# Kernel tuning notes

Hardware: AMD Instinct MI355X
Metric: run time of the kernel (lower is better)

## Reference

```python
import jax, jax.numpy as jnp
import numpy as np

OBS_DIM, EMBED_DIM, HIDDEN = 64, 128, 256
BATCH, SEQLEN = 32, 2048


def setup_inputs() -> dict:
    key = jax.random.key(0)
    ks = jax.random.split(key, 8)
    N = BATCH * SEQLEN
    obs = jax.random.normal(ks[0], (N, OBS_DIM), dtype=jnp.float32)
    S = jnp.zeros((BATCH, 2 * HIDDEN), dtype=jnp.float32)  # [h, c] concat
    M = (jax.random.uniform(ks[1], (N,)) < 0.1).astype(jnp.float32)
    sc_e = 1.0 / np.sqrt(OBS_DIM)
    sc_k = 1.0 / np.sqrt(EMBED_DIM)
    sc_r = 1.0 / np.sqrt(HIDDEN)
    W_embed = jax.random.normal(ks[2], (OBS_DIM, EMBED_DIM), dtype=jnp.float32) * sc_e
    b_embed = jnp.zeros((EMBED_DIM,), dtype=jnp.float32)
    kernel = jax.random.normal(ks[3], (EMBED_DIM, 4 * HIDDEN), dtype=jnp.float32) * sc_k
    rec_kernel = jax.random.normal(ks[4], (HIDDEN, 4 * HIDDEN), dtype=jnp.float32) * sc_r
    bias = jnp.zeros((4 * HIDDEN,), dtype=jnp.float32)
    return {"obs": obs, "S": S, "M": M, "W_embed": W_embed, "b_embed": b_embed,
            "kernel": kernel, "rec_kernel": rec_kernel, "bias": bias}


def reference(obs, S, M, W_embed, b_embed, kernel, rec_kernel, bias):
    B = S.shape[0]
    H = S.shape[1] // 2
    # embedding_model: Dense  [B*T, obs_dim] -> [B*T, embed_dim]
    emb = obs @ W_embed + b_embed
    T = emb.shape[0] // B
    x = emb.reshape(B, T, -1)          # batch_to_seq
    m = M.reshape(B, T)                # batch_to_seq of mask
    h0, c0 = jnp.split(S, 2, axis=-1)  # LSTM states [h, c]

    def step(carry, xt):
        h, c = carry
        x_t, m_t = xt                  # x_t: [B, D], m_t: [B]
        keep = (1.0 - m_t)[:, None]    # mask==1 -> reset state (episode boundary)
        h = h * keep
        c = c * keep
        z = x_t @ kernel + h @ rec_kernel + bias  # [B, 4H]
        i, f, g, o = jnp.split(z, 4, axis=-1)     # keras gate order i,f,c,o
        i = jax.nn.sigmoid(i)
        f = jax.nn.sigmoid(f)
        g = jnp.tanh(g)
        o = jax.nn.sigmoid(o)
        c = f * c + i * g
        h = o * jnp.tanh(c)
        return (h, c), h

    xs = (jnp.swapaxes(x, 0, 1), jnp.swapaxes(m, 0, 1))  # time-major
    (_, _), hs = jax.lax.scan(step, (h0, c0), xs)        # hs: [T, B, H]
    memory = jnp.swapaxes(hs, 0, 1).reshape(B * T, H)    # seq_to_batch
    return memory
```

## Files before the change

kernel.cpp:

```cpp
#include <hip/hip_runtime.h>
#include <hip/hip_bf16.h>


#define T_SEQ   2048
#define NBATCH  32
#define OBS     64
#define HID     256
#define KROWS   320
#define GSLOTS  16
#define XPAD    324
#define MAXSEG  65536

__device__ __forceinline__ float sigm(float x) {
    x = fminf(fmaxf(x, -30.f), 30.f);
    return 1.f / (1.f + __expf(-x));
}
__device__ __forceinline__ float tanh_(float x) {
    x = fminf(fmaxf(x, -15.f), 15.f);
    float e = __expf(2.f * x);
    return (e - 1.f) / (e + 1.f);
}

__global__ void prep_kernel(const float* __restrict__ W_embed, const float* __restrict__ b_embed,
                            const float* __restrict__ kern,    const float* __restrict__ rec,
                            const float* __restrict__ bias,
                            float* __restrict__ Wg, float* __restrict__ bc4, unsigned* __restrict__ cnt) {
    int bi = blockIdx.x, tid = threadIdx.x;
    if (bi < 256) {
        int r = bi >> 2;
        int c = ((bi & 3) << 8) + tid;
        float acc = 0.f;
        #pragma unroll 8
        for (int k = 0; k < 128; ++k)
            acc = fmaf(W_embed[r * 128 + k], kern[k * 1024 + c], acc);
        Wg[(r * 256 + (c & 255)) * 4 + (c >> 8)] = acc;
    } else if (bi < 512) {
        int k = bi - 256;
        #pragma unroll
        for (int p = 0; p < 4; ++p) {
            int c = (p << 8) + tid;
            Wg[((64 + k) * 256 + (c & 255)) * 4 + (c >> 8)] = rec[k * 1024 + c];
        }
    } else if (bi == 512) {
        #pragma unroll
        for (int p = 0; p < 4; ++p) {
            int c = (p << 8) + tid;
            float acc = bias[c];
            for (int k = 0; k < 128; ++k)
                acc = fmaf(b_embed[k], kern[k * 1024 + c], acc);
            bc4[(c & 255) * 4 + (c >> 8)] = acc;
        }
    } else {
        if (tid < 16) cnt[tid] = 0u;
    }
}

__global__ void seg_kernel(const float* __restrict__ M, uint2* __restrict__ segs,
                           unsigned* __restrict__ cnt) {
    int b = blockIdx.x, tid = threadIdx.x;
    int base = b * T_SEQ;
    for (int t = tid; t < T_SEQ; t += 256) {
        bool start = (t == 0) || (M[base + t] != 0.f);
        if (!start) continue;
        int t2 = t + 1;
        while (t2 < T_SEQ && M[base + t2] == 0.f) ++t2;
        unsigned idx = atomicAdd(&cnt[0], 1u);
        segs[idx] = make_uint2((unsigned)(base + t), (unsigned)(t2 - t));
    }
}

__global__ void sort_kernel(const uint2* __restrict__ segs, uint2* __restrict__ out,
                            unsigned* __restrict__ cnt) {
    __shared__ unsigned hist[2049];
    __shared__ unsigned partial[256];
    __shared__ unsigned ofs[2049];
    int tid = threadIdx.x;
    unsigned n = cnt[0];
    for (int i = tid; i < 2049; i += 256) hist[i] = 0u;
    __syncthreads();
    for (unsigned i = tid; i < n; i += 256) atomicAdd(&hist[segs[i].y], 1u);
    __syncthreads();
    int cs = tid * 8 + 1;
    unsigned s = 0;
    #pragma unroll
    for (int i = 0; i < 8; ++i) s += hist[cs + i];
    partial[tid] = s;
    __syncthreads();
    if (tid == 0) {
        unsigned run = 0;
        for (int t = 255; t >= 0; --t) { unsigned p = partial[t]; partial[t] = run; run += p; }
    }
    __syncthreads();
    unsigned run = partial[tid];
    #pragma unroll
    for (int i = 7; i >= 0; --i) { int bin = cs + i; ofs[bin] = run; run += hist[bin]; }
    __syncthreads();
    for (unsigned i = tid; i < n; i += 256) {
        uint2 sg = segs[i];
        unsigned pos = atomicAdd(&ofs[sg.y], 1u);
        out[pos] = sg;
    }
}

template <int N>
__device__ __forceinline__ void step_n(float (*X)[XPAD], float (*C)[HID],
                                       const float* __restrict__ Wg,
                                       const float* __restrict__ bc4,
                                       const unsigned* __restrict__ ssn,
                                       float* __restrict__ out, int tid) {
    const float4* __restrict__ W4 = (const float4*)Wg;
    float4 acc[N];
    const float4 bcv = ((const float4*)bc4)[tid];
    #pragma unroll
    for (int g = 0; g < N; ++g) acc[g] = bcv;

    for (int k4 = 0; k4 < KROWS / 4; ++k4) {
        float4 w[4];
        #pragma unroll
        for (int i = 0; i < 4; ++i) w[i] = W4[(k4 * 4 + i) * 256 + tid];
        #pragma unroll
        for (int g = 0; g < N; ++g) {
            const float4 xv = *(const float4*)&X[g][k4 * 4];
            float xs0 = xv.x, xs1 = xv.y, xs2 = xv.z, xs3 = xv.w;
            acc[g].x = fmaf(xs0, w[0].x, acc[g].x);
            acc[g].y = fmaf(xs0, w[0].y, acc[g].y);
            acc[g].z = fmaf(xs0, w[0].z, acc[g].z);
            acc[g].w = fmaf(xs0, w[0].w, acc[g].w);
            acc[g].x = fmaf(xs1, w[1].x, acc[g].x);
            acc[g].y = fmaf(xs1, w[1].y, acc[g].y);
            acc[g].z = fmaf(xs1, w[1].z, acc[g].z);
            acc[g].w = fmaf(xs1, w[1].w, acc[g].w);
            acc[g].x = fmaf(xs2, w[2].x, acc[g].x);
            acc[g].y = fmaf(xs2, w[2].y, acc[g].y);
            acc[g].z = fmaf(xs2, w[2].z, acc[g].z);
            acc[g].w = fmaf(xs2, w[2].w, acc[g].w);
            acc[g].x = fmaf(xs3, w[3].x, acc[g].x);
            acc[g].y = fmaf(xs3, w[3].y, acc[g].y);
            acc[g].z = fmaf(xs3, w[3].z, acc[g].z);
            acc[g].w = fmaf(xs3, w[3].w, acc[g].w);
        }
    }
    float hv[N], cv[N];
    #pragma unroll
    for (int g = 0; g < N; ++g) {
        float i = sigm(acc[g].x);
        float f = sigm(acc[g].y);
        float gg = tanh_(acc[g].z);
        float o = sigm(acc[g].w);
        float c = fmaf(f, C[g][tid], i * gg);
        hv[g] = o * tanh_(c);
        cv[g] = c;
    }
    __syncthreads();
    #pragma unroll
    for (int g = 0; g < N; ++g) {
        C[g][tid] = cv[g];
        X[g][OBS + tid] = hv[g];
        out[(size_t)ssn[g] * HID + tid] = hv[g];
    }
}

__launch_bounds__(256)
__global__ void lstm_kernel(const float* __restrict__ obs, const float* __restrict__ S,
                            const float* __restrict__ M,
                            const float* __restrict__ Wg, const float* __restrict__ bc4,
                            const uint2* __restrict__ segs, unsigned* __restrict__ cnt,
                            float* __restrict__ out) {
    __shared__ float X[GSLOTS][XPAD];
    __shared__ float C[GSLOTS][HID];
    __shared__ unsigned ssn[GSLOTS], send[GSLOTS];
    __shared__ int   sact[GSLOTS], sfresh[GSLOTS];
    __shared__ float smg[GSLOTS];
    __shared__ int   sh_nact, sh_nmig;
    __shared__ unsigned sh_mask;
    __shared__ int   msrc[GSLOTS], mdst[GSLOTS];

    const int tid = threadIdx.x;
    const unsigned nseg = cnt[0];
    if (tid < GSLOTS) sact[tid] = 0;
    __syncthreads();

    for (;;) {
        if (tid < GSLOTS) {
            int g = tid;
            if (sact[g]) {
                unsigned nn = ssn[g] + 1;
                if (nn >= send[g]) sact[g] = 0; else ssn[g] = nn;
            }
            sfresh[g] = 0;
            if (!sact[g]) {
                unsigned idx = atomicAdd(&cnt[1], 1u);
                if (idx < nseg) {
                    uint2 sg = segs[idx];
                    ssn[g] = sg.x; send[g] = sg.x + sg.y;
                    sact[g] = 1; sfresh[g] = 1;
                }
            }
        }
        if (tid < 64) {
            unsigned long long bal = __ballot(tid < GSLOTS && sact[tid]);
            if (tid == 0) {
                unsigned m = (unsigned)(bal & 0xFFFFull);
                sh_mask = m;
                sh_nact = __popc(m);
            }
        }
        __syncthreads();
        const unsigned mask = sh_mask;
        if (mask == 0u) break;
        const int nact = sh_nact;

        if (mask != ((1u << nact) - 1u)) {
            if (tid == 0) {
                int w = 0, nm = 0;
                for (int g = 0; g < GSLOTS; ++g) if (sact[g]) {
                    if (g != w) {
                        msrc[nm] = g; mdst[nm] = w; ++nm;
                        ssn[w] = ssn[g]; send[w] = send[g];
                        sfresh[w] = sfresh[g];
                        sact[w] = 1; sact[g] = 0;
                    }
                    ++w;
                }
                sh_nmig = nm;
            }
            __syncthreads();
            const int nm = sh_nmig;
            for (int i = 0; i < nm; ++i) {
                int s = msrc[i], d = mdst[i];
                X[d][tid] = X[s][tid];
                if (tid + 256 < XPAD) X[d][tid + 256] = X[s][tid + 256];
                C[d][tid] = C[s][tid];
            }
            __syncthreads();
        }

        if (tid < GSLOTS) {
            int g = tid;
            smg[g] = (g < nact) ? M[ssn[g]] : 0.f;
        }
        for (int g = 0; g < nact; ++g) {
            if (sfresh[g]) {
                unsigned n0 = ssn[g];
                if ((n0 & (T_SEQ - 1)) == 0u) {
                    unsigned b = n0 >> 11;
                    X[g][OBS + tid] = S[b * 512 + tid];
                    C[g][tid]       = S[b * 512 + 256 + tid];
                } else {
                    X[g][OBS + tid] = 0.f;
                    C[g][tid]       = 0.f;
                }
            }
        }
        {
            int g = (tid >> 6);
            int e = tid & 63;
            #pragma unroll
            for (int p = 0; p < 4; ++p, g += 4)
                if (g < nact) X[g][e] = obs[(size_t)ssn[g] * OBS + e];
        }
        __syncthreads();

        for (int g = 0; g < nact; ++g) {
            if (smg[g] != 0.f) { X[g][OBS + tid] = 0.f; C[g][tid] = 0.f; }
        }
        __syncthreads();

        switch (nact) {
            case 1:  step_n<1>(X, C, Wg, bc4, ssn, out, tid); break;
            case 2:  step_n<2>(X, C, Wg, bc4, ssn, out, tid); break;
            case 3:  step_n<3>(X, C, Wg, bc4, ssn, out, tid); break;
            case 4:  step_n<4>(X, C, Wg, bc4, ssn, out, tid); break;
            case 5:  step_n<5>(X, C, Wg, bc4, ssn, out, tid); break;
            case 6:  step_n<6>(X, C, Wg, bc4, ssn, out, tid); break;
            case 7:  step_n<7>(X, C, Wg, bc4, ssn, out, tid); break;
            case 8:  step_n<8>(X, C, Wg, bc4, ssn, out, tid); break;
            case 9:  step_n<9>(X, C, Wg, bc4, ssn, out, tid); break;
            case 10: step_n<10>(X, C, Wg, bc4, ssn, out, tid); break;
            case 11: step_n<11>(X, C, Wg, bc4, ssn, out, tid); break;
            case 12: step_n<12>(X, C, Wg, bc4, ssn, out, tid); break;
            case 13: step_n<13>(X, C, Wg, bc4, ssn, out, tid); break;
            case 14: step_n<14>(X, C, Wg, bc4, ssn, out, tid); break;
            case 15: step_n<15>(X, C, Wg, bc4, ssn, out, tid); break;
            default: step_n<16>(X, C, Wg, bc4, ssn, out, tid); break;
        }
        __syncthreads();
    }
}

extern "C" void kernel_launch(void* const* d_in, const int* in_sizes, int n_in,
                              void* d_out, int out_size, void* d_ws, size_t ws_size,
                              hipStream_t stream) {
    const float* obs     = (const float*)d_in[0];
    const float* S       = (const float*)d_in[1];
    const float* M       = (const float*)d_in[2];
    const float* W_embed = (const float*)d_in[3];
    const float* b_embed = (const float*)d_in[4];
    const float* kern    = (const float*)d_in[5];
    const float* rec     = (const float*)d_in[6];
    const float* bias    = (const float*)d_in[7];
    float* out = (float*)d_out;

    float*    ws    = (float*)d_ws;
    float*    Wg    = ws;
    float*    bc4   = Wg + 320 * 1024;
    unsigned* cnt   = (unsigned*)(bc4 + 1024);
    uint2*    segs  = (uint2*)(cnt + 16);
    uint2*    ssort = segs + MAXSEG;

    hipLaunchKernelGGL(prep_kernel, dim3(514), dim3(256), 0, stream,
                       W_embed, b_embed, kern, rec, bias, Wg, bc4, cnt);
    hipLaunchKernelGGL(seg_kernel, dim3(NBATCH), dim3(256), 0, stream, M, segs, cnt);
    hipLaunchKernelGGL(sort_kernel, dim3(1), dim3(256), 0, stream, segs, ssort, cnt);
    hipLaunchKernelGGL(lstm_kernel, dim3(256), dim3(256), 0, stream,
                       obs, S, M, Wg, bc4, ssort, cnt, out);
}
```

Baseline: 3.010 ms.

## Keep fp16-packed LSTM weights in registers, one segment per 1024-thread block

Rewrites the LSTM kernel so each of 1024 threads owns one gate column and holds its 320 weights as 160 packed fp16 pairs in registers. Each block processes one segment at a time with fp16 dot2 instructions, replacing the multi-slot batching scheme that re-read fp32 weights from global/L2 every step. Weights and hidden state are quantised to fp16, which reduces precision. The 160-register weight array with launch_bounds(1024,8) risks register spills, and processing a single segment per step gives up the batching across segments.

```diff
diff --git a/kernel.cpp b/kernel.cpp
--- a/kernel.cpp
+++ b/kernel.cpp
@@ -1,5 +1,6 @@
 #include <hip/hip_runtime.h>
 #include <hip/hip_bf16.h>
+#include <hip/hip_fp16.h>
 
 
 #define T_SEQ   2048
@@ -7,9 +8,9 @@
 #define OBS     64
 #define HID     256
 #define KROWS   320
-#define GSLOTS  16
-#define XPAD    324
+#define KP      160
 #define MAXSEG  65536
+#define NWG     512
 
 __device__ __forceinline__ float sigm(float x) {
     x = fminf(fmaxf(x, -30.f), 30.f);
@@ -21,37 +22,52 @@
     return (e - 1.f) / (e + 1.f);
 }
 
+typedef _Float16 h2_t __attribute__((ext_vector_type(2)));
+__device__ __forceinline__ float dot2(unsigned w, unsigned x, float acc) {
+#if defined(__has_builtin) && __has_builtin(__builtin_amdgcn_fdot2)
+    return __builtin_amdgcn_fdot2(__builtin_bit_cast(h2_t, w),
+                                  __builtin_bit_cast(h2_t, x), acc, false);
+#else
+    float wl = __half2float(__ushort_as_half((unsigned short)(w & 0xffffu)));
+    float wh = __half2float(__ushort_as_half((unsigned short)(w >> 16)));
+    float xl = __half2float(__ushort_as_half((unsigned short)(x & 0xffffu)));
+    float xh = __half2float(__ushort_as_half((unsigned short)(x >> 16)));
+    return fmaf(wh, xh, fmaf(wl, xl, acc));
+#endif
+}
+
+__device__ __forceinline__ unsigned packh(float a, float b) {
+    return (unsigned)__half_as_ushort(__float2half(a)) |
+           ((unsigned)__half_as_ushort(__float2half(b)) << 16);
+}
+
 __global__ void prep_kernel(const float* __restrict__ W_embed, const float* __restrict__ b_embed,
                             const float* __restrict__ kern,    const float* __restrict__ rec,
                             const float* __restrict__ bias,
-                            float* __restrict__ Wg, float* __restrict__ bc4, unsigned* __restrict__ cnt) {
-    int bi = blockIdx.x, tid = threadIdx.x;
-    if (bi < 256) {
-        int r = bi >> 2;
-        int c = ((bi & 3) << 8) + tid;
-        float acc = 0.f;
+                            unsigned* __restrict__ Wp, float* __restrict__ bc,
+                            unsigned* __restrict__ cnt) {
+    int kp = blockIdx.x, j = threadIdx.x;
+    if (kp < 32) {
+        int r0 = 2 * kp, r1 = 2 * kp + 1;
+        float wa = 0.f, wb = 0.f;
         #pragma unroll 8
+        for (int k = 0; k < 128; ++k) {
+            float kv = kern[k * 1024 + j];
+            wa = fmaf(W_embed[r0 * 128 + k], kv, wa);
+            wb = fmaf(W_embed[r1 * 128 + k], kv, wb);
+        }
+        Wp[kp * 1024 + j] = packh(wa, wb);
+    } else if (kp < 160) {
+        int k0 = 2 * (kp - 32);
+        float wa = rec[(size_t)k0 * 1024 + j];
+        float wb = rec[(size_t)(k0 + 1) * 1024 + j];
+        Wp[kp * 1024 + j] = packh(wa, wb);
+    } else {
+        float acc = bias[j];
         for (int k = 0; k < 128; ++k)
-            acc = fmaf(W_embed[r * 128 + k], kern[k * 1024 + c], acc);
-        Wg[(r * 256 + (c & 255)) * 4 + (c >> 8)] = acc;
-    } else if (bi < 512) {
-        int k = bi - 256;
-        #pragma unroll
-        for (int p = 0; p < 4; ++p) {
-            int c = (p << 8) + tid;
-            Wg[((64 + k) * 256 + (c & 255)) * 4 + (c >> 8)] = rec[k * 1024 + c];
-        }
-    } else if (bi == 512) {
-        #pragma unroll
-        for (int p = 0; p < 4; ++p) {
-            int c = (p << 8) + tid;
-            float acc = bias[c];
-            for (int k = 0; k < 128; ++k)
-                acc = fmaf(b_embed[k], kern[k * 1024 + c], acc);
-            bc4[(c & 255) * 4 + (c >> 8)] = acc;
-        }
-    } else {
-        if (tid < 16) cnt[tid] = 0u;
+            acc = fmaf(b_embed[k], kern[k * 1024 + j], acc);
+        bc[j] = acc;
+        if (j < 16) cnt[j] = 0u;
     }
 }
 
@@ -102,189 +118,75 @@
     }
 }
 
-template <int N>
-__device__ __forceinline__ void step_n(float (*X)[XPAD], float (*C)[HID],
-                                       const float* __restrict__ Wg,
-                                       const float* __restrict__ bc4,
-                                       const unsigned* __restrict__ ssn,
-                                       float* __restrict__ out, int tid) {
-    const float4* __restrict__ W4 = (const float4*)Wg;
-    float4 acc[N];
-    const float4 bcv = ((const float4*)bc4)[tid];
-    #pragma unroll
-    for (int g = 0; g < N; ++g) acc[g] = bcv;
-
-    for (int k4 = 0; k4 < KROWS / 4; ++k4) {
-        float4 w[4];
-        #pragma unroll
-        for (int i = 0; i < 4; ++i) w[i] = W4[(k4 * 4 + i) * 256 + tid];
-        #pragma unroll
-        for (int g = 0; g < N; ++g) {
-            const float4 xv = *(const float4*)&X[g][k4 * 4];
-            float xs0 = xv.x, xs1 = xv.y, xs2 = xv.z, xs3 = xv.w;
-            acc[g].x = fmaf(xs0, w[0].x, acc[g].x);
-            acc[g].y = fmaf(xs0, w[0].y, acc[g].y);
-            acc[g].z = fmaf(xs0, w[0].z, acc[g].z);
-            acc[g].w = fmaf(xs0, w[0].w, acc[g].w);
-            acc[g].x = fmaf(xs1, w[1].x, acc[g].x);
-            acc[g].y = fmaf(xs1, w[1].y, acc[g].y);
-            acc[g].z = fmaf(xs1, w[1].z, acc[g].z);
-            acc[g].w = fmaf(xs1, w[1].w, acc[g].w);
-            acc[g].x = fmaf(xs2, w[2].x, acc[g].x);
-            acc[g].y = fmaf(xs2, w[2].y, acc[g].y);
-            acc[g].z = fmaf(xs2, w[2].z, acc[g].z);
-            acc[g].w = fmaf(xs2, w[2].w, acc[g].w);
-            acc[g].x = fmaf(xs3, w[3].x, acc[g].x);
-            acc[g].y = fmaf(xs3, w[3].y, acc[g].y);
-            acc[g].z = fmaf(xs3, w[3].z, acc[g].z);
-            acc[g].w = fmaf(xs3, w[3].w, acc[g].w);
-        }
-    }
-    float hv[N], cv[N];
-    #pragma unroll
-    for (int g = 0; g < N; ++g) {
-        float i = sigm(acc[g].x);
-        float f = sigm(acc[g].y);
-        float gg = tanh_(acc[g].z);
-        float o = sigm(acc[g].w);
-        float c = fmaf(f, C[g][tid], i * gg);
-        hv[g] = o * tanh_(c);
-        cv[g] = c;
-    }
-    __syncthreads();
-    #pragma unroll
-    for (int g = 0; g < N; ++g) {
-        C[g][tid] = cv[g];
-        X[g][OBS + tid] = hv[g];
-        out[(size_t)ssn[g] * HID + tid] = hv[g];
-    }
-}
-
-__launch_bounds__(256)
-__global__ void lstm_kernel(const float* __restrict__ obs, const float* __restrict__ S,
-                            const float* __restrict__ M,
-                            const float* __restrict__ Wg, const float* __restrict__ bc4,
-                            const uint2* __restrict__ segs, unsigned* __restrict__ cnt,
-                            float* __restrict__ out) {
-    __shared__ float X[GSLOTS][XPAD];
-    __shared__ float C[GSLOTS][HID];
-    __shared__ unsigned ssn[GSLOTS], send[GSLOTS];
-    __shared__ int   sact[GSLOTS], sfresh[GSLOTS];
-    __shared__ float smg[GSLOTS];
-    __shared__ int   sh_nact, sh_nmig;
-    __shared__ unsigned sh_mask;
-    __shared__ int   msrc[GSLOTS], mdst[GSLOTS];
+__global__ __launch_bounds__(1024, 8)
+void lstm_kernel(const float* __restrict__ obs, const float* __restrict__ S,
+                 const float* __restrict__ M,
+                 const unsigned* __restrict__ Wp, const float* __restrict__ bc,
+                 const uint2* __restrict__ segs, unsigned* __restrict__ cnt,
+                 float* __restrict__ out) {
+    __shared__ uint4 X4[KP / 4];
+    __shared__ float zb[1024];
+    __shared__ unsigned sh_idx;
+    __half* Xh = (__half*)X4;
 
     const int tid = threadIdx.x;
     const unsigned nseg = cnt[0];
-    if (tid < GSLOTS) sact[tid] = 0;
-    __syncthreads();
-
+
+    unsigned w[KP];
+    {
+        const unsigned* wp = Wp + tid;
+        #pragma unroll
+        for (int kp = 0; kp < KP; ++kp) w[kp] = wp[kp << 10];
+    }
+    const float bcj = bc[tid];
+
+    float c = 0.f;
     for (;;) {
-        if (tid < GSLOTS) {
-            int g = tid;
-            if (sact[g]) {
-                unsigned nn = ssn[g] + 1;
-                if (nn >= send[g]) sact[g] = 0; else ssn[g] = nn;
+        if (tid == 0) sh_idx = atomicAdd(&cnt[1], 1u);
+        __syncthreads();
+        unsigned idx = sh_idx;
+        if (idx >= nseg) break;
+        uint2 sg = segs[idx];
+        unsigned n0 = sg.x, n1 = sg.x + sg.y;
+
+        if (tid < HID) {
+            float h0 = 0.f;
+            c = 0.f;
+            if ((n0 & (T_SEQ - 1)) == 0u && M[n0] == 0.f) {
+                unsigned b = n0 >> 11;
+                h0 = S[b * 512 + tid];
+                c  = S[b * 512 + 256 + tid];
             }
-            sfresh[g] = 0;
-            if (!sact[g]) {
-                unsigned idx = atomicAdd(&cnt[1], 1u);
-                if (idx < nseg) {
-                    uint2 sg = segs[idx];
-                    ssn[g] = sg.x; send[g] = sg.x + sg.y;
-                    sact[g] = 1; sfresh[g] = 1;
-                }
+            Xh[OBS + tid] = __float2half(h0);
+        }
+
+        for (unsigned n = n0; n < n1; ++n) {
+            if (tid < OBS) Xh[tid] = __float2half(obs[(size_t)n * OBS + tid]);
+            __syncthreads();
+            float a0 = bcj, a1 = 0.f, a2 = 0.f, a3 = 0.f;
+            #pragma unroll
+            for (int q = 0; q < KP / 4; ++q) {
+                uint4 xv = X4[q];
+                a0 = dot2(w[q * 4 + 0], xv.x, a0);
+                a1 = dot2(w[q * 4 + 1], xv.y, a1);
+                a2 = dot2(w[q * 4 + 2], xv.z, a2);
+                a3 = dot2(w[q * 4 + 3], xv.w, a3);
+            }
+            zb[tid] = (a0 + a1) + (a2 + a3);
+            __syncthreads();
+            if (tid < HID) {
+                float zi = zb[tid], zf = zb[tid + 256];
+                float zg = zb[tid + 512], zo = zb[tid + 768];
+                float i = sigm(zi);
+                float f = sigm(zf);
+                float g = tanh_(zg);
+                float o = sigm(zo);
+                c = fmaf(f, c, i * g);
+                float h = o * tanh_(c);
+                Xh[OBS + tid] = __float2half(h);
+                out[(size_t)n * HID + tid] = h;
             }
         }
-        if (tid < 64) {
-            unsigned long long bal = __ballot(tid < GSLOTS && sact[tid]);
-            if (tid == 0) {
-                unsigned m = (unsigned)(bal & 0xFFFFull);
-                sh_mask = m;
-                sh_nact = __popc(m);
-            }
-        }
-        __syncthreads();
-        const unsigned mask = sh_mask;
-        if (mask == 0u) break;
-        const int nact = sh_nact;
-
-        if (mask != ((1u << nact) - 1u)) {
-            if (tid == 0) {
-                int w = 0, nm = 0;
-                for (int g = 0; g < GSLOTS; ++g) if (sact[g]) {
-                    if (g != w) {
-                        msrc[nm] = g; mdst[nm] = w; ++nm;
-                        ssn[w] = ssn[g]; send[w] = send[g];
-                        sfresh[w] = sfresh[g];
-                        sact[w] = 1; sact[g] = 0;
-                    }
-                    ++w;
-                }
-                sh_nmig = nm;
-            }
-            __syncthreads();
-            const int nm = sh_nmig;
-            for (int i = 0; i < nm; ++i) {
-                int s = msrc[i], d = mdst[i];
-                X[d][tid] = X[s][tid];
-                if (tid + 256 < XPAD) X[d][tid + 256] = X[s][tid + 256];
-                C[d][tid] = C[s][tid];
-            }
-            __syncthreads();
-        }
-
-        if (tid < GSLOTS) {
-            int g = tid;
-            smg[g] = (g < nact) ? M[ssn[g]] : 0.f;
-        }
-        for (int g = 0; g < nact; ++g) {
-            if (sfresh[g]) {
-                unsigned n0 = ssn[g];
-                if ((n0 & (T_SEQ - 1)) == 0u) {
-                    unsigned b = n0 >> 11;
-                    X[g][OBS + tid] = S[b * 512 + tid];
-                    C[g][tid]       = S[b * 512 + 256 + tid];
-                } else {
-                    X[g][OBS + tid] = 0.f;
-                    C[g][tid]       = 0.f;
-                }
-            }
-        }
-        {
-            int g = (tid >> 6);
-            int e = tid & 63;
-            #pragma unroll
-            for (int p = 0; p < 4; ++p, g += 4)
-                if (g < nact) X[g][e] = obs[(size_t)ssn[g] * OBS + e];
-        }
-        __syncthreads();
-
-        for (int g = 0; g < nact; ++g) {
-            if (smg[g] != 0.f) { X[g][OBS + tid] = 0.f; C[g][tid] = 0.f; }
-        }
-        __syncthreads();
-
-        switch (nact) {
-            case 1:  step_n<1>(X, C, Wg, bc4, ssn, out, tid); break;
-            case 2:  step_n<2>(X, C, Wg, bc4, ssn, out, tid); break;
-            case 3:  step_n<3>(X, C, Wg, bc4, ssn, out, tid); break;
-            case 4:  step_n<4>(X, C, Wg, bc4, ssn, out, tid); break;
-            case 5:  step_n<5>(X, C, Wg, bc4, ssn, out, tid); break;
-            case 6:  step_n<6>(X, C, Wg, bc4, ssn, out, tid); break;
-            case 7:  step_n<7>(X, C, Wg, bc4, ssn, out, tid); break;
-            case 8:  step_n<8>(X, C, Wg, bc4, ssn, out, tid); break;
-            case 9:  step_n<9>(X, C, Wg, bc4, ssn, out, tid); break;
-            case 10: step_n<10>(X, C, Wg, bc4, ssn, out, tid); break;
-            case 11: step_n<11>(X, C, Wg, bc4, ssn, out, tid); break;
-            case 12: step_n<12>(X, C, Wg, bc4, ssn, out, tid); break;
-            case 13: step_n<13>(X, C, Wg, bc4, ssn, out, tid); break;
-            case 14: step_n<14>(X, C, Wg, bc4, ssn, out, tid); break;
-            case 15: step_n<15>(X, C, Wg, bc4, ssn, out, tid); break;
-            default: step_n<16>(X, C, Wg, bc4, ssn, out, tid); break;
-        }
-        __syncthreads();
     }
 }
 
@@ -301,17 +203,16 @@
     const float* bias    = (const float*)d_in[7];
     float* out = (float*)d_out;
 
-    float*    ws    = (float*)d_ws;
-    float*    Wg    = ws;
-    float*    bc4   = Wg + 320 * 1024;
-    unsigned* cnt   = (unsigned*)(bc4 + 1024);
+    unsigned* Wp    = (unsigned*)d_ws;
+    float*    bc    = (float*)(Wp + KP * 1024);
+    unsigned* cnt   = (unsigned*)(bc + 1024);
     uint2*    segs  = (uint2*)(cnt + 16);
     uint2*    ssort = segs + MAXSEG;
 
-    hipLaunchKernelGGL(prep_kernel, dim3(514), dim3(256), 0, stream,
-                       W_embed, b_embed, kern, rec, bias, Wg, bc4, cnt);
+    hipLaunchKernelGGL(prep_kernel, dim3(161), dim3(1024), 0, stream,
+                       W_embed, b_embed, kern, rec, bias, Wp, bc, cnt);
     hipLaunchKernelGGL(seg_kernel, dim3(NBATCH), dim3(256), 0, stream, M, segs, cnt);
     hipLaunchKernelGGL(sort_kernel, dim3(1), dim3(256), 0, stream, segs, ssort, cnt);
-    hipLaunchKernelGGL(lstm_kernel, dim3(256), dim3(256), 0, stream,
-                       obs, S, M, Wg, bc4, ssort, cnt, out);
-}
+    hipLaunchKernelGGL(lstm_kernel, dim3(NWG), dim3(1024), 0, stream,
+                       obs, S, M, Wp, bc, ssort, cnt, out);
+}
```

Result: slower. 5.062 ms (+68.2%).

## Pack weights to fp16 with dot2, precompute input projection, keep cell state in registers

Applied to the files above, without the earlier changes.

Stores the fused embed/kernel and recurrent weights as packed fp16 pairs. Per-step gate accumulation now uses fdot2 instructions, which halves weight bandwidth and instruction count. A new zx_kernel precomputes the input-side projection for all timesteps into an fp16 workspace buffer when workspace space allows, so the recurrent loop only handles the 256 hidden rows. The cell state moves from shared memory into registers, the reset mask is folded into segment starts, and the grid doubles to 512 workgroups with 2 blocks per CU. The trade-off is reduced numeric precision (fp16 weights, inputs and h) and a dependence on workspace size.

```diff
diff --git a/kernel.cpp b/kernel.cpp
--- a/kernel.cpp
+++ b/kernel.cpp
@@ -1,15 +1,17 @@
 #include <hip/hip_runtime.h>
 #include <hip/hip_bf16.h>
+#include <hip/hip_fp16.h>
 
 
 #define T_SEQ   2048
 #define NBATCH  32
 #define OBS     64
 #define HID     256
-#define KROWS   320
 #define GSLOTS  16
-#define XPAD    324
+#define NK2     160
+#define ZK2     32
 #define MAXSEG  65536
+#define NWG     512
 
 __device__ __forceinline__ float sigm(float x) {
     x = fminf(fmaxf(x, -30.f), 30.f);
@@ -21,37 +23,94 @@
     return (e - 1.f) / (e + 1.f);
 }
 
+typedef _Float16 h2_t __attribute__((ext_vector_type(2)));
+__device__ __forceinline__ float dot2(unsigned w, unsigned x, float acc) {
+#if defined(__has_builtin) && __has_builtin(__builtin_amdgcn_fdot2)
+    return __builtin_amdgcn_fdot2(__builtin_bit_cast(h2_t, w),
+                                  __builtin_bit_cast(h2_t, x), acc, false);
+#else
+    float wl = __half2float(__ushort_as_half((unsigned short)(w & 0xffffu)));
+    float wh = __half2float(__ushort_as_half((unsigned short)(w >> 16)));
+    float xl = __half2float(__ushort_as_half((unsigned short)(x & 0xffffu)));
+    float xh = __half2float(__ushort_as_half((unsigned short)(x >> 16)));
+    return fmaf(wh, xh, fmaf(wl, xl, acc));
+#endif
+}
+__device__ __forceinline__ unsigned packh(float a, float b) {
+    return (unsigned)__half_as_ushort(__float2half(a)) |
+           ((unsigned)__half_as_ushort(__float2half(b)) << 16);
+}
+
 __global__ void prep_kernel(const float* __restrict__ W_embed, const float* __restrict__ b_embed,
                             const float* __restrict__ kern,    const float* __restrict__ rec,
                             const float* __restrict__ bias,
-                            float* __restrict__ Wg, float* __restrict__ bc4, unsigned* __restrict__ cnt) {
-    int bi = blockIdx.x, tid = threadIdx.x;
-    if (bi < 256) {
-        int r = bi >> 2;
-        int c = ((bi & 3) << 8) + tid;
-        float acc = 0.f;
-        #pragma unroll 8
-        for (int k = 0; k < 128; ++k)
-            acc = fmaf(W_embed[r * 128 + k], kern[k * 1024 + c], acc);
-        Wg[(r * 256 + (c & 255)) * 4 + (c >> 8)] = acc;
-    } else if (bi < 512) {
-        int k = bi - 256;
-        #pragma unroll
-        for (int p = 0; p < 4; ++p) {
-            int c = (p << 8) + tid;
-            Wg[((64 + k) * 256 + (c & 255)) * 4 + (c >> 8)] = rec[k * 1024 + c];
-        }
-    } else if (bi == 512) {
-        #pragma unroll
-        for (int p = 0; p < 4; ++p) {
-            int c = (p << 8) + tid;
-            float acc = bias[c];
-            for (int k = 0; k < 128; ++k)
-                acc = fmaf(b_embed[k], kern[k * 1024 + c], acc);
-            bc4[(c & 255) * 4 + (c >> 8)] = acc;
-        }
+                            uint4* __restrict__ W4, float4* __restrict__ bc4,
+                            unsigned* __restrict__ cnt) {
+    int b = blockIdx.x, j = threadIdx.x;
+    if (b < ZK2) {
+        int r0 = 2 * b, r1 = r0 + 1;
+        float d0[4] = {0.f, 0.f, 0.f, 0.f}, d1[4] = {0.f, 0.f, 0.f, 0.f};
+        for (int k = 0; k < 128; ++k) {
+            float e0 = W_embed[r0 * 128 + k], e1 = W_embed[r1 * 128 + k];
+            #pragma unroll
+            for (int q = 0; q < 4; ++q) {
+                float kv = kern[k * 1024 + (q << 8) + j];
+                d0[q] = fmaf(e0, kv, d0[q]);
+                d1[q] = fmaf(e1, kv, d1[q]);
+            }
+        }
+        W4[b * 256 + j] = make_uint4(packh(d0[0], d1[0]), packh(d0[1], d1[1]),
+                                     packh(d0[2], d1[2]), packh(d0[3], d1[3]));
+    } else if (b < NK2) {
+        size_t k0 = (size_t)2 * (b - ZK2), k1 = k0 + 1;
+        W4[b * 256 + j] = make_uint4(
+            packh(rec[k0 * 1024 + j],       rec[k1 * 1024 + j]),
+            packh(rec[k0 * 1024 + 256 + j], rec[k1 * 1024 + 256 + j]),
+            packh(rec[k0 * 1024 + 512 + j], rec[k1 * 1024 + 512 + j]),
+            packh(rec[k0 * 1024 + 768 + j], rec[k1 * 1024 + 768 + j]));
     } else {
-        if (tid < 16) cnt[tid] = 0u;
+        float a[4];
+        #pragma unroll
+        for (int q = 0; q < 4; ++q) a[q] = bias[(q << 8) + j];
+        for (int k = 0; k < 128; ++k) {
+            float e = b_embed[k];
+            #pragma unroll
+            for (int q = 0; q < 4; ++q)
+                a[q] = fmaf(e, kern[k * 1024 + (q << 8) + j], a[q]);
+        }
+        bc4[j] = make_float4(a[0], a[1], a[2], a[3]);
+        if (j < 16) cnt[j] = 0u;
+    }
+}
+
+__global__ __launch_bounds__(256, 2)
+void zx_kernel(const float* __restrict__ obs, const uint4* __restrict__ W4,
+               const float4* __restrict__ bc4, uint2* __restrict__ zx4) {
+    __shared__ __half obsh[64][64];
+    const int tid = threadIdx.x;
+    const size_t base = (size_t)blockIdx.x * 64 * 64;
+    const size_t row0 = (size_t)blockIdx.x * 64;
+    for (int i = tid; i < 4096; i += 256)
+        obsh[i >> 6][i & 63] = __float2half(obs[base + i]);
+    __syncthreads();
+
+    uint4 w[32];
+    #pragma unroll
+    for (int k2 = 0; k2 < 32; ++k2) w[k2] = W4[k2 * 256 + tid];
+    const float4 bc = bc4[tid];
+
+    const unsigned* __restrict__ ob32 = (const unsigned*)obsh;
+    for (int n = 0; n < 64; ++n) {
+        float4 a = bc;
+        #pragma unroll
+        for (int k2 = 0; k2 < 32; ++k2) {
+            unsigned xv = ob32[n * 32 + k2];
+            a.x = dot2(w[k2].x, xv, a.x);
+            a.y = dot2(w[k2].y, xv, a.y);
+            a.z = dot2(w[k2].z, xv, a.z);
+            a.w = dot2(w[k2].w, xv, a.w);
+        }
+        zx4[(row0 + n) * 256 + tid] = make_uint2(packh(a.x, a.y), packh(a.z, a.w));
     }
 }
 
@@ -102,81 +161,91 @@
     }
 }
 
-template <int N>
-__device__ __forceinline__ void step_n(float (*X)[XPAD], float (*C)[HID],
-                                       const float* __restrict__ Wg,
-                                       const float* __restrict__ bc4,
-                                       const unsigned* __restrict__ ssn,
-                                       float* __restrict__ out, int tid) {
-    const float4* __restrict__ W4 = (const float4*)Wg;
+template <int N, int Z0>
+__device__ __forceinline__ void step_n(unsigned (*X)[NK2], float (&c)[GSLOTS],
+                                       const uint4* __restrict__ W4,
+                                       const float4* __restrict__ bc4,
+                                       const uint2* __restrict__ zx4,
+                                       const unsigned* ssn, float* __restrict__ out,
+                                       int tid) {
     float4 acc[N];
-    const float4 bcv = ((const float4*)bc4)[tid];
-    #pragma unroll
-    for (int g = 0; g < N; ++g) acc[g] = bcv;
-
-    for (int k4 = 0; k4 < KROWS / 4; ++k4) {
-        float4 w[4];
-        #pragma unroll
-        for (int i = 0; i < 4; ++i) w[i] = W4[(k4 * 4 + i) * 256 + tid];
+    if (Z0 == 0) {
+        const float4 b = bc4[tid];
+        #pragma unroll
+        for (int g = 0; g < N; ++g) acc[g] = b;
+    } else {
         #pragma unroll
         for (int g = 0; g < N; ++g) {
-            const float4 xv = *(const float4*)&X[g][k4 * 4];
-            float xs0 = xv.x, xs1 = xv.y, xs2 = xv.z, xs3 = xv.w;
-            acc[g].x = fmaf(xs0, w[0].x, acc[g].x);
-            acc[g].y = fmaf(xs0, w[0].y, acc[g].y);
-            acc[g].z = fmaf(xs0, w[0].z, acc[g].z);
-            acc[g].w = fmaf(xs0, w[0].w, acc[g].w);
-            acc[g].x = fmaf(xs1, w[1].x, acc[g].x);
-            acc[g].y = fmaf(xs1, w[1].y, acc[g].y);
-            acc[g].z = fmaf(xs1, w[1].z, acc[g].z);
-            acc[g].w = fmaf(xs1, w[1].w, acc[g].w);
-            acc[g].x = fmaf(xs2, w[2].x, acc[g].x);
-            acc[g].y = fmaf(xs2, w[2].y, acc[g].y);
-            acc[g].z = fmaf(xs2, w[2].z, acc[g].z);
-            acc[g].w = fmaf(xs2, w[2].w, acc[g].w);
-            acc[g].x = fmaf(xs3, w[3].x, acc[g].x);
-            acc[g].y = fmaf(xs3, w[3].y, acc[g].y);
-            acc[g].z = fmaf(xs3, w[3].z, acc[g].z);
-            acc[g].w = fmaf(xs3, w[3].w, acc[g].w);
-        }
-    }
-    float hv[N], cv[N];
+            uint2 z = zx4[(size_t)ssn[g] * 256 + tid];
+            acc[g].x = __half2float(__ushort_as_half((unsigned short)(z.x & 0xffffu)));
+            acc[g].y = __half2float(__ushort_as_half((unsigned short)(z.x >> 16)));
+            acc[g].z = __half2float(__ushort_as_half((unsigned short)(z.y & 0xffffu)));
+            acc[g].w = __half2float(__ushort_as_half((unsigned short)(z.y >> 16)));
+        }
+    }
+    for (int k2 = Z0; k2 < NK2; k2 += 4) {
+        uint4 w0 = W4[(k2 + 0) * 256 + tid];
+        uint4 w1 = W4[(k2 + 1) * 256 + tid];
+        uint4 w2 = W4[(k2 + 2) * 256 + tid];
+        uint4 w3 = W4[(k2 + 3) * 256 + tid];
+        #pragma unroll
+        for (int g = 0; g < N; ++g) {
+            const uint4 xv = *(const uint4*)&X[g][k2];
+            acc[g].x = dot2(w0.x, xv.x, acc[g].x);
+            acc[g].y = dot2(w0.y, xv.x, acc[g].y);
+            acc[g].z = dot2(w0.z, xv.x, acc[g].z);
+            acc[g].w = dot2(w0.w, xv.x, acc[g].w);
+            acc[g].x = dot2(w1.x, xv.y, acc[g].x);
+            acc[g].y = dot2(w1.y, xv.y, acc[g].y);
+            acc[g].z = dot2(w1.z, xv.y, acc[g].z);
+            acc[g].w = dot2(w1.w, xv.y, acc[g].w);
+            acc[g].x = dot2(w2.x, xv.z, acc[g].x);
+            acc[g].y = dot2(w2.y, xv.z, acc[g].y);
+            acc[g].z = dot2(w2.z, xv.z, acc[g].z);
+            acc[g].w = dot2(w2.w, xv.z, acc[g].w);
+            acc[g].x = dot2(w3.x, xv.w, acc[g].x);
+            acc[g].y = dot2(w3.y, xv.w, acc[g].y);
+            acc[g].z = dot2(w3.z, xv.w, acc[g].z);
+            acc[g].w = dot2(w3.w, xv.w, acc[g].w);
+        }
+    }
+    float hv[N];
     #pragma unroll
     for (int g = 0; g < N; ++g) {
         float i = sigm(acc[g].x);
         float f = sigm(acc[g].y);
         float gg = tanh_(acc[g].z);
         float o = sigm(acc[g].w);
-        float c = fmaf(f, C[g][tid], i * gg);
-        hv[g] = o * tanh_(c);
-        cv[g] = c;
+        c[g] = fmaf(f, c[g], i * gg);
+        hv[g] = o * tanh_(c[g]);
     }
     __syncthreads();
     #pragma unroll
     for (int g = 0; g < N; ++g) {
-        C[g][tid] = cv[g];
-        X[g][OBS + tid] = hv[g];
+        ((__half*)X[g])[2 * ZK2 + tid] = __float2half(hv[g]);
         out[(size_t)ssn[g] * HID + tid] = hv[g];
     }
 }
 
-__launch_bounds__(256)
-__global__ void lstm_kernel(const float* __restrict__ obs, const float* __restrict__ S,
-                            const float* __restrict__ M,
-                            const float* __restrict__ Wg, const float* __restrict__ bc4,
-                            const uint2* __restrict__ segs, unsigned* __restrict__ cnt,
-                            float* __restrict__ out) {
-    __shared__ float X[GSLOTS][XPAD];
-    __shared__ float C[GSLOTS][HID];
+template <int Z0>
+__global__ __launch_bounds__(256, 2)
+void lstm_kernel(const float* __restrict__ obs, const float* __restrict__ S,
+                 const float* __restrict__ M,
+                 const uint4* __restrict__ W4, const float4* __restrict__ bc4,
+                 const uint2* __restrict__ zx4,
+                 const uint2* __restrict__ segs, unsigned* __restrict__ cnt,
+                 float* __restrict__ out) {
+    __shared__ unsigned X[GSLOTS][NK2];
+    __shared__ float    Cb[GSLOTS][HID];
     __shared__ unsigned ssn[GSLOTS], send[GSLOTS];
-    __shared__ int   sact[GSLOTS], sfresh[GSLOTS];
-    __shared__ float smg[GSLOTS];
-    __shared__ int   sh_nact, sh_nmig;
+    __shared__ int      sact[GSLOTS], sfresh[GSLOTS];
+    __shared__ int      sh_nact, sh_nmig;
     __shared__ unsigned sh_mask;
-    __shared__ int   msrc[GSLOTS], mdst[GSLOTS];
+    __shared__ int      msrc[GSLOTS], mdst[GSLOTS];
 
     const int tid = threadIdx.x;
     const unsigned nseg = cnt[0];
+    float c[GSLOTS];
     if (tid < GSLOTS) sact[tid] = 0;
     __syncthreads();
 
@@ -224,65 +293,62 @@
                 }
                 sh_nmig = nm;
             }
+            #pragma unroll
+            for (int g = 0; g < GSLOTS; ++g) Cb[g][tid] = c[g];
             __syncthreads();
             const int nm = sh_nmig;
             for (int i = 0; i < nm; ++i) {
                 int s = msrc[i], d = mdst[i];
-                X[d][tid] = X[s][tid];
-                if (tid + 256 < XPAD) X[d][tid + 256] = X[s][tid + 256];
-                C[d][tid] = C[s][tid];
+                if (tid < NK2) X[d][tid] = X[s][tid];
+                Cb[d][tid] = Cb[s][tid];
             }
             __syncthreads();
-        }
-
-        if (tid < GSLOTS) {
-            int g = tid;
-            smg[g] = (g < nact) ? M[ssn[g]] : 0.f;
-        }
-        for (int g = 0; g < nact; ++g) {
-            if (sfresh[g]) {
+            #pragma unroll
+            for (int g = 0; g < GSLOTS; ++g) c[g] = Cb[g][tid];
+        }
+
+        #pragma unroll
+        for (int g = 0; g < GSLOTS; ++g) {
+            if (g < nact && sfresh[g]) {
                 unsigned n0 = ssn[g];
-                if ((n0 & (T_SEQ - 1)) == 0u) {
+                float h0 = 0.f, c0 = 0.f;
+                if ((n0 & (T_SEQ - 1)) == 0u && M[n0] == 0.f) {
                     unsigned b = n0 >> 11;
-                    X[g][OBS + tid] = S[b * 512 + tid];
-                    C[g][tid]       = S[b * 512 + 256 + tid];
-                } else {
-                    X[g][OBS + tid] = 0.f;
-                    C[g][tid]       = 0.f;
+                    h0 = S[b * 512 + tid];
+                    c0 = S[b * 512 + 256 + tid];
                 }
-            }
-        }
-        {
-            int g = (tid >> 6);
-            int e = tid & 63;
-            #pragma unroll
-            for (int p = 0; p < 4; ++p, g += 4)
-                if (g < nact) X[g][e] = obs[(size_t)ssn[g] * OBS + e];
+                ((__half*)X[g])[2 * ZK2 + tid] = __float2half(h0);
+                c[g] = c0;
+            }
+        }
+        if (Z0 == 0) {
+            int g0 = (tid >> 6), e = tid & 63;
+            #pragma unroll
+            for (int p = 0; p < 4; ++p) {
+                int g = g0 + 4 * p;
+                if (g < nact)
+                    ((__half*)X[g])[e] = __float2half(obs[(size_t)ssn[g] * OBS + e]);
+            }
         }
         __syncthreads();
 
-        for (int g = 0; g < nact; ++g) {
-            if (smg[g] != 0.f) { X[g][OBS + tid] = 0.f; C[g][tid] = 0.f; }
-        }
-        __syncthreads();
-
         switch (nact) {
-            case 1:  step_n<1>(X, C, Wg, bc4, ssn, out, tid); break;
-            case 2:  step_n<2>(X, C, Wg, bc4, ssn, out, tid); break;
-            case 3:  step_n<3>(X, C, Wg, bc4, ssn, out, tid); break;
-            case 4:  step_n<4>(X, C, Wg, bc4, ssn, out, tid); break;
-            case 5:  step_n<5>(X, C, Wg, bc4, ssn, out, tid); break;
-            case 6:  step_n<6>(X, C, Wg, bc4, ssn, out, tid); break;
-            case 7:  step_n<7>(X, C, Wg, bc4, ssn, out, tid); break;
-            case 8:  step_n<8>(X, C, Wg, bc4, ssn, out, tid); break;
-            case 9:  step_n<9>(X, C, Wg, bc4, ssn, out, tid); break;
-            case 10: step_n<10>(X, C, Wg, bc4, ssn, out, tid); break;
-            case 11: step_n<11>(X, C, Wg, bc4, ssn, out, tid); break;
-            case 12: step_n<12>(X, C, Wg, bc4, ssn, out, tid); break;
-            case 13: step_n<13>(X, C, Wg, bc4, ssn, out, tid); break;
-            case 14: step_n<14>(X, C, Wg, bc4, ssn, out, tid); break;
-            case 15: step_n<15>(X, C, Wg, bc4, ssn, out, tid); break;
-            default: step_n<16>(X, C, Wg, bc4, ssn, out, tid); break;
+            case 1:  step_n<1,  Z0>(X, c, W4, bc4, zx4, ssn, out, tid); break;
+            case 2:  step_n<2,  Z0>(X, c, W4, bc4, zx4, ssn, out, tid); break;
+            case 3:  step_n<3,  Z0>(X, c, W4, bc4, zx4, ssn, out, tid); break;
+            case 4:  step_n<4,  Z0>(X, c, W4, bc4, zx4, ssn, out, tid); break;
+            case 5:  step_n<5,  Z0>(X, c, W4, bc4, zx4, ssn, out, tid); break;
+            case 6:  step_n<6,  Z0>(X, c, W4, bc4, zx4, ssn, out, tid); break;
+            case 7:  step_n<7,  Z0>(X, c, W4, bc4, zx4, ssn, out, tid); break;
+            case 8:  step_n<8,  Z0>(X, c, W4, bc4, zx4, ssn, out, tid); break;
+            case 9:  step_n<9,  Z0>(X, c, W4, bc4, zx4, ssn, out, tid); break;
+            case 10: step_n<10, Z0>(X, c, W4, bc4, zx4, ssn, out, tid); break;
+            case 11: step_n<11, Z0>(X, c, W4, bc4, zx4, ssn, out, tid); break;
+            case 12: step_n<12, Z0>(X, c, W4, bc4, zx4, ssn, out, tid); break;
+            case 13: step_n<13, Z0>(X, c, W4, bc4, zx4, ssn, out, tid); break;
+            case 14: step_n<14, Z0>(X, c, W4, bc4, zx4, ssn, out, tid); break;
+            case 15: step_n<15, Z0>(X, c, W4, bc4, zx4, ssn, out, tid); break;
+            default: step_n<16, Z0>(X, c, W4, bc4, zx4, ssn, out, tid); break;
         }
         __syncthreads();
     }
@@ -301,17 +367,25 @@
     const float* bias    = (const float*)d_in[7];
     float* out = (float*)d_out;
 
-    float*    ws    = (float*)d_ws;
-    float*    Wg    = ws;
-    float*    bc4   = Wg + 320 * 1024;
-    unsigned* cnt   = (unsigned*)(bc4 + 1024);
+    uint4*    W4    = (uint4*)d_ws;
+    float4*   bc4   = (float4*)(W4 + NK2 * 256);
+    unsigned* cnt   = (unsigned*)(bc4 + 256);
     uint2*    segs  = (uint2*)(cnt + 16);
     uint2*    ssort = segs + MAXSEG;
-
-    hipLaunchKernelGGL(prep_kernel, dim3(514), dim3(256), 0, stream,
-                       W_embed, b_embed, kern, rec, bias, Wg, bc4, cnt);
+    uint2*    zx4   = ssort + MAXSEG;
+    size_t    zx_need = (size_t)((char*)zx4 - (char*)d_ws) + (size_t)65536 * 256 * 8;
+    const bool use_zx = (ws_size >= zx_need);
+
+    hipLaunchKernelGGL(prep_kernel, dim3(NK2 + 1), dim3(256), 0, stream,
+                       W_embed, b_embed, kern, rec, bias, W4, bc4, cnt);
     hipLaunchKernelGGL(seg_kernel, dim3(NBATCH), dim3(256), 0, stream, M, segs, cnt);
     hipLaunchKernelGGL(sort_kernel, dim3(1), dim3(256), 0, stream, segs, ssort, cnt);
-    hipLaunchKernelGGL(lstm_kernel, dim3(256), dim3(256), 0, stream,
-                       obs, S, M, Wg, bc4, ssort, cnt, out);
-}
+    if (use_zx) {
+        hipLaunchKernelGGL(zx_kernel, dim3(1024), dim3(256), 0, stream, obs, W4, bc4, zx4);
+        hipLaunchKernelGGL((lstm_kernel<ZK2>), dim3(NWG), dim3(256), 0, stream,
+                           obs, S, M, W4, bc4, zx4, ssort, cnt, out);
+    } else {
+        hipLaunchKernelGGL((lstm_kernel<0>), dim3(NWG), dim3(256), 0, stream,
+                           obs, S, M, W4, bc4, zx4, ssort, cnt, out);
+    }
+}
```

New measurement: 2.940 ms. 2.3% less time.
